# Performance work log

Hardware: AMD Instinct MI355X
Metric: run time of the kernel (lower is better)

## Reference

```python
import jax, jax.numpy as jnp
import numpy as np

B, S, IN, H, D, NH, L, C = 32, 512, 3, 64, 128, 8, 4, 5
NSUB = 10          # euler substeps per interval: dt = interval/10 for these inputs
MAX_CONSEC = 50    # max_consecutive_steps in torch code
DH = D // NH
EPS = 1e-5


def _ln(x, g, b):
    m = x.mean(-1, keepdims=True)
    v = ((x - m) ** 2).mean(-1, keepdims=True)
    return (x - m) / jnp.sqrt(v + EPS) * g + b


def setup_inputs():
    key = jax.random.key(0)
    ks = jax.random.split(key, 24)
    def g(i, shape, scale=0.05):
        return jax.random.normal(ks[i], shape, dtype=jnp.float32) * scale
    dts = jax.random.uniform(ks[0], (B, S), minval=0.001, maxval=0.05, dtype=jnp.float32)
    times = jnp.cumsum(dts, axis=1)  # strictly increasing, positive
    return dict(
        time_series=jax.random.normal(ks[1], (B, S, IN), dtype=jnp.float32),
        times=times,
        noise=jax.random.normal(ks[2], (S, NSUB, B, H), dtype=jnp.float32),
        mask=jnp.ones((B, S), dtype=bool),
        enc_w=g(3, (IN, H)), enc_b=jnp.zeros((H,)),
        enc_g=jnp.ones((H,)), enc_beta=jnp.zeros((H,)),
        dw1=g(4, (H + 1, 2 * H)), db1=jnp.zeros((2 * H,)),
        dw2=g(5, (2 * H, H)), db2=jnp.zeros((H,)),
        dw3=g(6, (H, H)), db3=jnp.zeros((H,)),
        aw1=g(7, (1, H)), ab1=jnp.zeros((H,)),
        aw2=g(8, (H, H)), ab2=jnp.zeros((H,)),
        bw1=g(9, (1, H)), bb1=jnp.zeros((H,)),
        bw2=g(10, (H, H)), bb2=jnp.zeros((H,)),
        min_diff=jnp.float32(0.1),
        in_w=g(11, (H, D)), in_b=jnp.zeros((D,)),
        wq=g(12, (L, D, D)), bq=jnp.zeros((L, D)),
        wk=g(13, (L, D, D)), bk=jnp.zeros((L, D)),
        wv=g(14, (L, D, D)), bv=jnp.zeros((L, D)),
        wo=g(15, (L, D, D)), bo=jnp.zeros((L, D)),
        ln1_g=jnp.ones((L, D)), ln1_b=jnp.zeros((L, D)),
        ln2_g=jnp.ones((L, D)), ln2_b=jnp.zeros((L, D)),
        fw1=g(16, (L, D, 4 * D)), fb1=jnp.zeros((L, 4 * D)),
        fw2=g(17, (L, 4 * D, D)), fb2=jnp.zeros((L, D)),
        cw1=g(18, (D, D // 2)), cb1=jnp.zeros((D // 2,)),
        cw2=g(19, (D // 2, C)), cb2=jnp.zeros((C,)),
    )


def reference(time_series, times, noise, mask, enc_w, enc_b, enc_g, enc_beta,
              dw1, db1, dw2, db2, dw3, db3, aw1, ab1, aw2, ab2, bw1, bb1, bw2, bb2,
              min_diff, in_w, in_b, wq, bq, wk, bk, wv, bv, wo, bo,
              ln1_g, ln1_b, ln2_g, ln2_b, fw1, fb1, fw2, fb2, cw1, cb1, cw2, cb2):
    # feature encoder: Linear -> LayerNorm -> ReLU (dropout off / eval)
    enc = jax.nn.relu(_ln(time_series @ enc_w + enc_b, enc_g, enc_beta))  # (B,S,H)

    def drift(t, y):
        tcol = jnp.full((y.shape[0], 1), t, dtype=y.dtype)
        ty = jnp.concatenate([y, tcol], axis=1)
        h1 = jnp.tanh(ty @ dw1 + db1)
        h2 = jnp.tanh(h1 @ dw2 + db2)
        return h2 @ dw3 + db3

    def diffusion(t, y):
        tcol = jnp.full((y.shape[0], 1), t, dtype=y.dtype)
        A = jax.nn.softplus(jnp.tanh(tcol @ aw1 + ab1) @ aw2 + ab2)
        Bt = jnp.tanh(jnp.tanh(tcol @ bw1 + bb1) @ bw2 + bb2)
        return A + Bt * y + jnp.abs(min_diff)

    t_seq = times[0]  # torch code uses batch element 0's timestamps for sdeint

    def step(carry, xs):
        state, consec = carry
        enc_i, t_prev, t_cur, dW = xs  # dW: (NSUB,B,H) standard normals
        h = (t_cur - t_prev) / NSUB    # dt = interval/10 (< self.dt for these inputs)
        sqh = jnp.sqrt(h)
        y0 = jax.lax.stop_gradient(state)  # torch detaches y0 at every step

        def sub(y, kw):
            k, dw = kw
            t = t_prev + k * h
            return y + drift(t, y) * h + diffusion(t, y) * sqh * dw, None

        y_int, _ = jax.lax.scan(sub, y0, (jnp.arange(NSUB, dtype=jnp.float32), dW))
        skip = consec >= MAX_CONSEC
        out = jnp.where(skip, enc_i, y_int)
        consec = jnp.where(skip, jnp.int32(0), consec + 1)
        return (out, consec), out

    y0 = enc[:, 0]
    xs = (jnp.swapaxes(enc, 0, 1)[1:], t_seq[:-1], t_seq[1:], noise[1:])
    _, traj = jax.lax.scan(step, (y0, jnp.int32(0)), xs)
    sde_features = jnp.concatenate([y0[:, None], jnp.swapaxes(traj, 0, 1)], axis=1)  # (B,S,H)

    mf = mask.astype(sde_features.dtype)
    sde_features = sde_features * mf[..., None]  # MaskedSequenceProcessor.apply_mask

    # ContiFormer (post-LN transformer encoder) over SDE features
    x = sde_features @ in_w + in_b  # (B,S,D)
    neg = jnp.asarray(-1e9, x.dtype)
    for l in range(L):
        q = (x @ wq[l] + bq[l]).reshape(B, S, NH, DH)
        k = (x @ wk[l] + bk[l]).reshape(B, S, NH, DH)
        v = (x @ wv[l] + bv[l]).reshape(B, S, NH, DH)
        scores = jnp.einsum('bqhd,bkhd->bhqk', q, k) / np.float32(np.sqrt(DH))
        scores = jnp.where(mask[:, None, None, :], scores, neg)
        att = jax.nn.softmax(scores, axis=-1)
        o = jnp.einsum('bhqk,bkhd->bqhd', att, v).reshape(B, S, D) @ wo[l] + bo[l]
        x = _ln(x + o, ln1_g[l], ln1_b[l])
        f = jax.nn.relu(x @ fw1[l] + fb1[l]) @ fw2[l] + fb2[l]
        x = _ln(x + f, ln2_g[l], ln2_b[l])
    pooled = (x * mf[..., None]).sum(1) / jnp.maximum(mf.sum(1, keepdims=True), 1.0)

    logits = jax.nn.relu(pooled @ cw1 + cb1) @ cw2 + cb2
    return logits, sde_features
```

## Files before the change

kernel.cpp:

```cpp
#include <hip/hip_runtime.h>
#include <hip/hip_bf16.h>


typedef __attribute__((ext_vector_type(8))) short short8;
typedef __attribute__((ext_vector_type(4))) float f32x4;

static constexpr int OFF_TS      = 0;
static constexpr int OFF_TIMES   = 49152;
static constexpr int OFF_ENCW    = 65536;
static constexpr int OFF_ENCB    = 65728;
static constexpr int OFF_ENCG    = 65792;
static constexpr int OFF_ENCBETA = 65856;
static constexpr int OFF_DW1     = 65920;
static constexpr int OFF_DB1     = 74240;
static constexpr int OFF_DW2     = 74368;
static constexpr int OFF_DB2     = 82560;
static constexpr int OFF_DW3     = 82624;
static constexpr int OFF_DB3     = 86720;
static constexpr int OFF_AW1     = 86784;
static constexpr int OFF_AB1     = 86848;
static constexpr int OFF_AW2     = 86912;
static constexpr int OFF_AB2     = 91008;
static constexpr int OFF_BW1     = 91072;
static constexpr int OFF_BB1     = 91136;
static constexpr int OFF_BW2     = 91200;
static constexpr int OFF_BB2     = 95296;
static constexpr int OFF_MD      = 95360;
static constexpr int OFF_INW     = 95424;
static constexpr int OFF_INB     = 103616;
static constexpr int OFF_WQ      = 103744;
static constexpr int OFF_BQ      = 169280;
static constexpr int OFF_WK      = 169792;
static constexpr int OFF_BK      = 235328;
static constexpr int OFF_WV      = 235840;
static constexpr int OFF_BV      = 301376;
static constexpr int OFF_WO      = 301888;
static constexpr int OFF_BO      = 367424;
static constexpr int OFF_LN1G    = 367936;
static constexpr int OFF_LN1B    = 368448;
static constexpr int OFF_LN2G    = 368960;
static constexpr int OFF_LN2B    = 369472;
static constexpr int OFF_FW1     = 369984;
static constexpr int OFF_FB1     = 632128;
static constexpr int OFF_FW2     = 634176;
static constexpr int OFF_FB2     = 896320;
static constexpr int OFF_CW1     = 896832;
static constexpr int OFF_CB1     = 905024;
static constexpr int OFF_CW2     = 905088;
static constexpr int OFF_CB2     = 905472;
static constexpr int OFF_FLAG    = 905536;
static constexpr int OFF_ENC     = 905600;
static constexpr int OFF_COEFA   = 3002752;
static constexpr int OFF_COEFB   = 3329792;
static constexpr int OFF_B1C     = 3656832;
static constexpr int OFF_X       = 4310912;
static constexpr int OFF_XBF     = 6408064;
static constexpr int OFF_QKVBF   = 7456640;
static constexpr int OFF_OBF     = 10602368;
static constexpr int OFF_HBF     = 11650944;
static constexpr int OFF_SDEBF   = 15845248;
static constexpr int OFF_WQKVT   = 16369536;
static constexpr int OFF_WOT     = 16467840;
static constexpr int OFF_FW1T    = 16500608;
static constexpr int OFF_FW2T    = 16631680;
static constexpr int OFF_INWT    = 16762752;
static constexpr int OFF_BQKV    = 16766848;
static constexpr int OFF_TMP     = 23185280;

struct PtrPack { const void* p[45]; };

__device__ inline float wsum64(float v) {
#pragma unroll
  for (int off = 32; off > 0; off >>= 1) v += __shfl_xor(v, off, 64);
  return v;
}

__device__ inline float fast_tanh(float x) {
  x = fminf(fmaxf(x, -15.f), 15.f);
  float e = __expf(2.f * x);
  return (e - 1.f) / (e + 1.f);
}

__device__ inline float tanh5(float x) {
  float e = __builtin_amdgcn_exp2f(x * 2.88539008f);
  return 1.f - 2.f * __builtin_amdgcn_rcpf(e + 1.f);
}

__device__ inline float bfdec(unsigned short h) {
  return __uint_as_float(((unsigned)h) << 16);
}

__device__ inline short f2bf(float f) {
  unsigned u = __float_as_uint(f);
  return (short)((u + 0x7FFFu + ((u >> 16) & 1u)) >> 16);
}

__device__ inline void lds_barrier() {
  asm volatile("s_waitcnt lgkmcnt(0)\ns_barrier" ::: "memory");
}

__global__ __launch_bounds__(256) void ingest_kernel(PtrPack pk, float* __restrict__ W) {
  const int NE = 43;
  const int cnt[NE] = {49152,16384,192,64,64,64,8320,128,8192,64,4096,64,64,64,4096,64,
                       64,64,4096,64,1,8192,128,65536,512,65536,512,65536,512,65536,512,
                       512,512,512,512,262144,2048,262144,512,8192,64,320,5};
  const int src[NE] = {0,1,4,5,6,7,8,9,10,11,12,13,14,15,16,17,18,19,20,21,22,23,24,
                       25,26,27,28,29,30,31,32,33,34,35,36,37,38,39,40,41,42,43,44};
  const int dst[NE] = {OFF_TS,OFF_TIMES,OFF_ENCW,OFF_ENCB,OFF_ENCG,OFF_ENCBETA,OFF_DW1,
                       OFF_DB1,OFF_DW2,OFF_DB2,OFF_DW3,OFF_DB3,OFF_AW1,OFF_AB1,OFF_AW2,
                       OFF_AB2,OFF_BW1,OFF_BB1,OFF_BW2,OFF_BB2,OFF_MD,OFF_INW,OFF_INB,
                       OFF_WQ,OFF_BQ,OFF_WK,OFF_BK,OFF_WV,OFF_BV,OFF_WO,OFF_BO,
                       OFF_LN1G,OFF_LN1B,OFF_LN2G,OFF_LN2B,OFF_FW1,OFF_FB1,OFF_FW2,
                       OFF_FB2,OFF_CW1,OFF_CB1,OFF_CW2,OFF_CB2};
  const unsigned* eg = (const unsigned*)pk.p[6];
  int gmode = (eg[0] == 0x3F803F80u) ? 1 : 0;

  __shared__ int isbf[NE];
  if (threadIdx.x < NE) {
    int k = threadIdx.x;
    int f = gmode;
    if (gmode) {
      const unsigned short* us = (const unsigned short*)pk.p[src[k]];
      int n = cnt[k] < 32 ? cnt[k] : 32;
      for (int i = 0; i < n; ++i) {
        unsigned short h = us[i];
        if (h & 0x7FFF) {
          float a = fabsf(bfdec(h));
          if (!(a > 1e-20f && a < 1e4f)) { f = 0; break; }
        }
      }
    }
    isbf[k] = f;
  }
  __syncthreads();

  int gid = blockIdx.x * 256 + threadIdx.x;
  int stride = gridDim.x * 256;
  if (gid == 0) {
    int nf = gmode;
    if (gmode) {
      const unsigned short* us = (const unsigned short*)pk.p[2];
      for (int i = 0; i < 32; ++i) {
        unsigned short h = us[i];
        if (h & 0x7FFF) {
          float a = fabsf(bfdec(h));
          if (!(a > 1e-20f && a < 1e4f)) { nf = 0; break; }
        }
      }
    }
    ((int*)W)[OFF_FLAG] = nf;
  }
  for (int k = 0; k < NE; ++k) {
    int n = cnt[k];
    float* dp = W + dst[k];
    if (isbf[k]) {
      const unsigned short* us = (const unsigned short*)pk.p[src[k]];
      for (int e = gid; e < n; e += stride) dp[e] = bfdec(us[e]);
    } else {
      const float* fs = (const float*)pk.p[src[k]];
      for (int e = gid; e < n; e += stride) dp[e] = fs[e];
    }
  }
}

__global__ __launch_bounds__(128) void prelude_kernel(float* __restrict__ W,
                                                      float* __restrict__ outf) {
  int blk = blockIdx.x;
  int tid = threadIdx.x;
  if (blk < 5110) {
    int bi = blk;
    int step = bi / 10, k = bi - step * 10;
    float t_prev = W[OFF_TIMES + step];
    float t_cur  = W[OFF_TIMES + step + 1];
    float h = (t_cur - t_prev) * 0.1f;
    float t = t_prev + (float)k * h;
    __shared__ float av[64], bv[64];
    if (tid < 64) av[tid] = fast_tanh(t * W[OFF_AW1 + tid] + W[OFF_AB1 + tid]);
    else { int j = tid - 64; bv[j] = fast_tanh(t * W[OFF_BW1 + j] + W[OFF_BB1 + j]); }
    __syncthreads();
    if (tid < 64) {
      float a = W[OFF_AB2 + tid];
      for (int i = 0; i < 64; ++i) a += av[i] * W[OFF_AW2 + i*64 + tid];
      W[OFF_COEFA + bi*64 + tid] = fmaxf(a, 0.f) + log1pf(__expf(-fabsf(a)));
    } else {
      int j = tid - 64;
      float a = W[OFF_BB2 + j];
      for (int i = 0; i < 64; ++i) a += bv[i] * W[OFF_BW2 + i*64 + j];
      W[OFF_COEFB + bi*64 + j] = fast_tanh(a);
    }
    W[OFF_B1C + bi*128 + tid] = t * W[OFF_DW1 + 64*128 + tid] + W[OFF_DB1 + tid];
  } else if (blk < 5462) {
    if (tid >= 64) return;
    int idx = blk - 5110;
    int b = idx / 11, gi = idx - b*11;
    int row = b*512 + gi*51;
    int j = tid;
    float t0 = W[OFF_TS + row*3 + 0];
    float t1 = W[OFF_TS + row*3 + 1];
    float t2 = W[OFF_TS + row*3 + 2];
    float v = W[OFF_ENCB + j] + t0 * W[OFF_ENCW + j] + t1 * W[OFF_ENCW + 64 + j]
            + t2 * W[OFF_ENCW + 128 + j];
    float mean = wsum64(v) * (1.f / 64.f);
    float d = v - mean;
    float var = wsum64(d * d) * (1.f / 64.f);
    float o = d * rsqrtf(var + 1e-5f) * W[OFF_ENCG + j] + W[OFF_ENCBETA + j];
    o = fmaxf(o, 0.f);
    W[OFF_ENC + row*64 + j] = o;
    ((short*)(W + OFF_SDEBF))[row*64 + j] = f2bf(o);
    outf[160 + row*64 + j] = o;
  } else {
    short* wqkvT = (short*)(W + OFF_WQKVT);
    short* woT   = (short*)(W + OFF_WOT);
    short* fw1T  = (short*)(W + OFF_FW1T);
    short* fw2T  = (short*)(W + OFF_FW2T);
    short* inwT  = (short*)(W + OFF_INWT);
    float* bqkv  = W + OFF_BQKV;
    int gid = (blk - 5462) * 128 + tid;
    int stride = 512 * 128;
    for (int e = gid; e < 4096; e += stride) W[OFF_TMP + e] = 0.f;
    for (int e = gid; e < 796160; e += stride) {
      if (e < 196608) {
        int l = e / 49152, r = e % 49152, n = r >> 7, k = r & 127;
        float v = (n < 128) ? W[OFF_WQ + l*16384 + k*128 + n]
                : (n < 256) ? W[OFF_WK + l*16384 + k*128 + (n - 128)]
                            : W[OFF_WV + l*16384 + k*128 + (n - 256)];
        wqkvT[e] = f2bf(v);
      } else if (e < 262144) {
        int t = e - 196608; int l = t / 16384, r = t % 16384, n = r >> 7, k = r & 127;
        woT[t] = f2bf(W[OFF_WO + l*16384 + k*128 + n]);
      } else if (e < 524288) {
        int t = e - 262144; int l = t / 65536, r = t % 65536, n = r >> 7, k = r & 127;
        fw1T[t] = f2bf(W[OFF_FW1 + l*65536 + k*512 + n]);
      } else if (e < 786432) {
        int t = e - 524288; int l = t / 65536, r = t % 65536, n = r >> 9, k = r & 511;
        fw2T[t] = f2bf(W[OFF_FW2 + l*65536 + k*128 + n]);
      } else if (e < 794624) {
        int t = e - 786432; int n = t >> 6, k = t & 63;
        inwT[t] = f2bf(W[OFF_INW + k*128 + n]);
      } else {
        int t = e - 794624; int l = t / 384, j = t % 384;
        bqkv[t] = (j < 128) ? W[OFF_BQ + l*128 + j]
                : (j < 256) ? W[OFF_BK + l*128 + (j - 128)]
                            : W[OFF_BV + l*128 + (j - 256)];
      }
    }
  }
}

__global__ __launch_bounds__(256, 1) void sde_kernel(float* __restrict__ W,
                                                     const void* __restrict__ noise,
                                                     float* __restrict__ outf) {
  __shared__ short ybf[16 * 72];
  __shared__ short h1bf[16 * 136];
  __shared__ short h2bf[16 * 72];

  const int tid = threadIdx.x;
  const int w   = tid >> 6;
  const int lane = tid & 63;
  const int q   = lane >> 4;
  const int lq  = lane & 15;
  const int g   = blockIdx.x >> 1;
  const int r0  = (blockIdx.x & 1) * 16;

  const int nmode = ((const int*)W)[OFF_FLAG];
  const float md = fabsf(W[OFF_MD]);
  const unsigned short* nb16 = (const unsigned short*)noise;
  const float* nf32 = (const float*)noise;
  short* sdebf = (short*)(W + OFF_SDEBF);

  const int ncol = w*16 + lq;
  short8 B1f[2][2];
#pragma unroll
  for (int kt = 0; kt < 2; ++kt)
#pragma unroll
    for (int ct = 0; ct < 2; ++ct)
#pragma unroll
      for (int j = 0; j < 8; ++j)
        B1f[kt][ct][j] = f2bf(W[OFF_DW1 + (kt*32 + q*8 + j)*128 + w*32 + ct*16 + lq]);
  short8 B2f[4];
#pragma unroll
  for (int kt = 0; kt < 4; ++kt)
#pragma unroll
    for (int j = 0; j < 8; ++j)
      B2f[kt][j] = f2bf(W[OFF_DW2 + (kt*32 + q*8 + j)*64 + ncol]);
  short8 B3f[2];
#pragma unroll
  for (int kt = 0; kt < 2; ++kt)
#pragma unroll
    for (int j = 0; j < 8; ++j)
      B3f[kt][j] = f2bf(W[OFF_DW3 + (kt*32 + q*8 + j)*64 + ncol]);
  const float db2v = W[OFF_DB2 + ncol];
  const float db3v = W[OFF_DB3 + ncol];

  float yreg[4];
#pragma unroll
  for (int r = 0; r < 4; ++r) {
    yreg[r] = W[OFF_ENC + ((r0 + q*4 + r)*512 + 51*g)*64 + ncol];
    ybf[(q*4 + r)*72 + ncol] = f2bf(yreg[r]);
  }

  const int ci0 = 51*g*10;
  float bias_a = W[OFF_B1C + ci0*128 + w*32 + lq];
  float bias_b = W[OFF_B1C + ci0*128 + w*32 + 16 + lq];
  float ca = W[OFF_COEFA + ci0*64 + ncol];
  float cb = W[OFF_COEFB + ci0*64 + ncol];

  const int nsteps = (g == 10) ? 1 : 50;
  for (int m = 0; m < nsteps; ++m) {
    const int istep = 51*g + m;
    const float t_prev = W[OFF_TIMES + istep];
    const float t_cur  = W[OFF_TIMES + istep + 1];
    const float hstep = (t_cur - t_prev) * 0.1f;
    const float sqh = sqrtf(hstep);
    for (int k = 0; k < 10; ++k) {
      const int ci = istep*10 + k;
      const int cin = (ci + 1 > 5109) ? 5109 : ci + 1;
      float b1na = W[OFF_B1C + cin*128 + w*32 + lq];
      float b1nb = W[OFF_B1C + cin*128 + w*32 + 16 + lq];
      float can = W[OFF_COEFA + cin*64 + ncol];
      float cbn = W[OFF_COEFB + cin*64 + ncol];
      float dwv[4];
      {
        const int nb = (((istep + 1)*10 + k)*32 + r0 + q*4)*64 + ncol;
#pragma unroll
        for (int r = 0; r < 4; ++r)
          dwv[r] = nmode ? bfdec(nb16[nb + r*64]) : nf32[nb + r*64];
      }
      lds_barrier();
      {
        short8 a0 = *(const short8*)&ybf[lq*72 + q*8];
        short8 a1 = *(const short8*)&ybf[lq*72 + 32 + q*8];
        f32x4 c0 = {bias_a, bias_a, bias_a, bias_a};
        c0 = __builtin_amdgcn_mfma_f32_16x16x32_bf16(a0, B1f[0][0], c0, 0, 0, 0);
        c0 = __builtin_amdgcn_mfma_f32_16x16x32_bf16(a1, B1f[1][0], c0, 0, 0, 0);
        f32x4 c1 = {bias_b, bias_b, bias_b, bias_b};
        c1 = __builtin_amdgcn_mfma_f32_16x16x32_bf16(a0, B1f[0][1], c1, 0, 0, 0);
        c1 = __builtin_amdgcn_mfma_f32_16x16x32_bf16(a1, B1f[1][1], c1, 0, 0, 0);
#pragma unroll
        for (int r = 0; r < 4; ++r) {
          h1bf[(q*4 + r)*136 + w*32 + lq]      = f2bf(tanh5(c0[r]));
          h1bf[(q*4 + r)*136 + w*32 + 16 + lq] = f2bf(tanh5(c1[r]));
        }
      }
      lds_barrier();
      {
        short8 h0 = *(const short8*)&h1bf[lq*136 + q*8];
        short8 h1 = *(const short8*)&h1bf[lq*136 + 32 + q*8];
        short8 h2 = *(const short8*)&h1bf[lq*136 + 64 + q*8];
        short8 h3 = *(const short8*)&h1bf[lq*136 + 96 + q*8];
        f32x4 cA = {db2v, db2v, db2v, db2v};
        cA = __builtin_amdgcn_mfma_f32_16x16x32_bf16(h0, B2f[0], cA, 0, 0, 0);
        cA = __builtin_amdgcn_mfma_f32_16x16x32_bf16(h1, B2f[1], cA, 0, 0, 0);
        f32x4 cB = {0.f, 0.f, 0.f, 0.f};
        cB = __builtin_amdgcn_mfma_f32_16x16x32_bf16(h2, B2f[2], cB, 0, 0, 0);
        cB = __builtin_amdgcn_mfma_f32_16x16x32_bf16(h3, B2f[3], cB, 0, 0, 0);
#pragma unroll
        for (int r = 0; r < 4; ++r)
          h2bf[(q*4 + r)*72 + ncol] = f2bf(tanh5(cA[r] + cB[r]));
      }
      lds_barrier();
      {
        short8 g0 = *(const short8*)&h2bf[lq*72 + q*8];
        short8 g1 = *(const short8*)&h2bf[lq*72 + 32 + q*8];
        f32x4 d = {db3v, db3v, db3v, db3v};
        d = __builtin_amdgcn_mfma_f32_16x16x32_bf16(g0, B3f[0], d, 0, 0, 0);
        d = __builtin_amdgcn_mfma_f32_16x16x32_bf16(g1, B3f[1], d, 0, 0, 0);
#pragma unroll
        for (int r = 0; r < 4; ++r) {
          float yv = yreg[r];
          yv = yv + d[r]*hstep + (ca + cb*yv + md)*sqh*dwv[r];
          yreg[r] = yv;
          ybf[(q*4 + r)*72 + ncol] = f2bf(yv);
        }
      }
      bias_a = b1na; bias_b = b1nb; ca = can; cb = cbn;
    }
#pragma unroll
    for (int r = 0; r < 4; ++r) {
      const int gi = ((r0 + q*4 + r)*512 + (istep + 1))*64 + ncol;
      sdebf[gi] = f2bf(yreg[r]);
      outf[160 + gi] = yreg[r];
    }
  }
}

__global__ __launch_bounds__(256) void gemm_ln64_kernel(
    const short* __restrict__ A, const short* __restrict__ BT,
    const float* __restrict__ bias, float* __restrict__ X,
    short* __restrict__ Xb, int K) {
  __shared__ short As[64 * 40];
  __shared__ short Bs[128 * 40];
  const int tid = threadIdx.x;
  const int w = tid >> 6, lane = tid & 63, q = lane >> 4, lq = lane & 15;
  const int bm = blockIdx.x * 64;
  f32x4 acc[8];
#pragma unroll
  for (int i = 0; i < 8; ++i) acc[i] = (f32x4){0.f, 0.f, 0.f, 0.f};

  const int arow = tid >> 2, acol = (tid & 3) * 8;
  const int brow = tid >> 1, bcol = (tid & 1) * 16;
  for (int k0 = 0; k0 < K; k0 += 32) {
    short8 a  = *(const short8*)&A[(bm + arow)*K + k0 + acol];
    short8 b0 = *(const short8*)&BT[brow*K + k0 + bcol];
    short8 b1 = *(const short8*)&BT[brow*K + k0 + bcol + 8];
    __syncthreads();
    *(short8*)&As[arow*40 + acol]    = a;
    *(short8*)&Bs[brow*40 + bcol]    = b0;
    *(short8*)&Bs[brow*40 + bcol+8]  = b1;
    __syncthreads();
    short8 af = *(const short8*)&As[(w*16 + lq)*40 + q*8];
#pragma unroll
    for (int ni = 0; ni < 8; ++ni) {
      short8 bf = *(const short8*)&Bs[(ni*16 + lq)*40 + q*8];
      acc[ni] = __builtin_amdgcn_mfma_f32_16x16x32_bf16(af, bf, acc[ni], 0, 0, 0);
    }
  }
#pragma unroll
  for (int r = 0; r < 4; ++r) {
    const int row = bm + w*16 + q*4 + r;
#pragma unroll
    for (int ni = 0; ni < 8; ++ni) {
      const int col = ni*16 + lq;
      float v = acc[ni][r] + bias[col];
      X[row*128 + col] = v;
      Xb[row*128 + col] = f2bf(v);
    }
  }
}

__global__ __launch_bounds__(512, 4) void ffn_fused_kernel(
    const short* __restrict__ Obf, const short* __restrict__ woT,
    const float* __restrict__ bo,
    const float* __restrict__ ln1g, const float* __restrict__ ln1b,
    const short* __restrict__ fw1T, const float* __restrict__ fb1,
    const short* __restrict__ fw2T, const float* __restrict__ fb2,
    const float* __restrict__ ln2g, const float* __restrict__ ln2b,
    float* __restrict__ X, short* __restrict__ Xb,
    float* __restrict__ psum) {
  __shared__ short U1[32 * 136];
  __shared__ short Hs[32 * 136];
  __shared__ short Bs[128 * 136];
  __shared__ float LNp[32][4][2];
  const int tid = threadIdx.x;
  const int w8 = tid >> 6, rg = w8 & 1, cq = w8 >> 1;
  const int lane = tid & 63, q = lane >> 4, lq = lane & 15;
  const int bm = blockIdx.x * 32;
  const int sr = tid >> 4, sc = (tid & 15) * 8;
  const int bn = tid >> 2, kb = (tid & 3) * 32;
  const int rowl0 = rg*16 + q*4;

  short8 abuf, bbuf[4];
  abuf = *(const short8*)&Obf[(bm + sr)*128 + sc];
#pragma unroll
  for (int j = 0; j < 4; ++j)
    bbuf[j] = *(const short8*)&woT[bn*128 + kb + j*8];
  *(short8*)&U1[sr*136 + sc] = abuf;
#pragma unroll
  for (int j = 0; j < 4; ++j) *(short8*)&Bs[bn*136 + kb + j*8] = bbuf[j];
  lds_barrier();

#pragma unroll
  for (int j = 0; j < 4; ++j)
    bbuf[j] = *(const short8*)&fw1T[bn*128 + kb + j*8];

  f32x4 acc[2];
#pragma unroll
  for (int i = 0; i < 2; ++i) acc[i] = (f32x4){0.f, 0.f, 0.f, 0.f};
#pragma unroll
  for (int ks = 0; ks < 4; ++ks) {
    short8 af = *(const short8*)&U1[(rg*16 + lq)*136 + ks*32 + q*8];
#pragma unroll
    for (int ni = 0; ni < 2; ++ni) {
      short8 bf = *(const short8*)&Bs[((cq*2 + ni)*16 + lq)*136 + ks*32 + q*8];
      acc[ni] = __builtin_amdgcn_mfma_f32_16x16x32_bf16(af, bf, acc[ni], 0, 0, 0);
    }
  }
  float vbuf[4][2];
#pragma unroll
  for (int r = 0; r < 4; ++r) {
    const int row = bm + rowl0 + r;
    float s = 0.f, s2 = 0.f;
#pragma unroll
    for (int ni = 0; ni < 2; ++ni) {
      const int col = cq*32 + ni*16 + lq;
      float t = acc[ni][r] + bo[col] + X[row*128 + col];
      vbuf[r][ni] = t; s += t; s2 += t*t;
    }
#pragma unroll
    for (int off = 1; off < 16; off <<= 1) {
      s  += __shfl_xor(s, off, 16);
      s2 += __shfl_xor(s2, off, 16);
    }
    if (lq == 0) { LNp[rowl0 + r][cq][0] = s; LNp[rowl0 + r][cq][1] = s2; }
  }
  lds_barrier();
#pragma unroll
  for (int j = 0; j < 4; ++j) *(short8*)&Bs[bn*136 + kb + j*8] = bbuf[j];
#pragma unroll
  for (int j = 0; j < 4; ++j)
    bbuf[j] = *(const short8*)&fw2T[bn*512 + kb + j*8];
  float xv[4][2];
#pragma unroll
  for (int r = 0; r < 4; ++r) {
    const int rowl = rowl0 + r;
    float s  = LNp[rowl][0][0] + LNp[rowl][1][0] + LNp[rowl][2][0] + LNp[rowl][3][0];
    float s2 = LNp[rowl][0][1] + LNp[rowl][1][1] + LNp[rowl][2][1] + LNp[rowl][3][1];
    float mean = s * (1.f / 128.f);
    float var = s2 * (1.f / 128.f) - mean * mean;
    float inv = rsqrtf(var + 1e-5f);
#pragma unroll
    for (int ni = 0; ni < 2; ++ni) {
      const int col = cq*32 + ni*16 + lq;
      float o = (vbuf[r][ni] - mean) * inv * ln1g[col] + ln1b[col];
      xv[r][ni] = o;
      U1[rowl*136 + col] = f2bf(o);
    }
  }
  lds_barrier();

  f32x4 acc2[2];
#pragma unroll
  for (int i = 0; i < 2; ++i) acc2[i] = (f32x4){0.f, 0.f, 0.f, 0.f};

  for (int c = 0; c < 4; ++c) {
#pragma unroll
    for (int i = 0; i < 2; ++i) acc[i] = (f32x4){0.f, 0.f, 0.f, 0.f};
#pragma unroll
    for (int ks = 0; ks < 4; ++ks) {
      short8 af = *(const short8*)&U1[(rg*16 + lq)*136 + ks*32 + q*8];
#pragma unroll
      for (int ni = 0; ni < 2; ++ni) {
        short8 bf = *(const short8*)&Bs[((cq*2 + ni)*16 + lq)*136 + ks*32 + q*8];
        acc[ni] = __builtin_amdgcn_mfma_f32_16x16x32_bf16(af, bf, acc[ni], 0, 0, 0);
      }
    }
#pragma unroll
    for (int r = 0; r < 4; ++r)
#pragma unroll
      for (int ni = 0; ni < 2; ++ni) {
        const int cl = cq*32 + ni*16 + lq;
        float hvv = fmaxf(acc[ni][r] + fb1[c*128 + cl], 0.f);
        Hs[(rowl0 + r)*136 + cl] = f2bf(hvv);
      }
    lds_barrier();
#pragma unroll
    for (int j = 0; j < 4; ++j) *(short8*)&Bs[bn*136 + kb + j*8] = bbuf[j];
    if (c < 3) {
#pragma unroll
      for (int j = 0; j < 4; ++j)
        bbuf[j] = *(const short8*)&fw1T[((c + 1)*128 + bn)*128 + kb + j*8];
    }
    lds_barrier();
#pragma unroll
    for (int ks = 0; ks < 4; ++ks) {
      short8 af = *(const short8*)&Hs[(rg*16 + lq)*136 + ks*32 + q*8];
#pragma unroll
      for (int ni = 0; ni < 2; ++ni) {
        short8 bf = *(const short8*)&Bs[((cq*2 + ni)*16 + lq)*136 + ks*32 + q*8];
        acc2[ni] = __builtin_amdgcn_mfma_f32_16x16x32_bf16(af, bf, acc2[ni], 0, 0, 0);
      }
    }
    if (c < 3) {
      lds_barrier();
#pragma unroll
      for (int j = 0; j < 4; ++j) *(short8*)&Bs[bn*136 + kb + j*8] = bbuf[j];
#pragma unroll
      for (int j = 0; j < 4; ++j)
        bbuf[j] = *(const short8*)&fw2T[bn*512 + (c + 1)*128 + kb + j*8];
      lds_barrier();
    }
  }

#pragma unroll
  for (int r = 0; r < 4; ++r) {
    float s = 0.f, s2 = 0.f;
#pragma unroll
    for (int ni = 0; ni < 2; ++ni) {
      const int col = cq*32 + ni*16 + lq;
      float t = acc2[ni][r] + fb2[col] + xv[r][ni];
      vbuf[r][ni] = t; s += t; s2 += t*t;
    }
#pragma unroll
    for (int off = 1; off < 16; off <<= 1) {
      s  += __shfl_xor(s, off, 16);
      s2 += __shfl_xor(s2, off, 16);
    }
    if (lq == 0) { LNp[rowl0 + r][cq][0] = s; LNp[rowl0 + r][cq][1] = s2; }
  }
  lds_barrier();
  float ps[2] = {0.f, 0.f};
#pragma unroll
  for (int r = 0; r < 4; ++r) {
    const int rowl = rowl0 + r;
    const int row = bm + rowl;
    float s  = LNp[rowl][0][0] + LNp[rowl][1][0] + LNp[rowl][2][0] + LNp[rowl][3][0];
    float s2 = LNp[rowl][0][1] + LNp[rowl][1][1] + LNp[rowl][2][1] + LNp[rowl][3][1];
    float mean = s * (1.f / 128.f);
    float var = s2 * (1.f / 128.f) - mean * mean;
    float inv = rsqrtf(var + 1e-5f);
#pragma unroll
    for (int ni = 0; ni < 2; ++ni) {
      const int col = cq*32 + ni*16 + lq;
      float o = (vbuf[r][ni] - mean) * inv * ln2g[col] + ln2b[col];
      X[row*128 + col] = o;
      Xb[row*128 + col] = f2bf(o);
      ps[ni] += o;
    }
  }
  if (psum != nullptr) {
    const int b = bm >> 9;
#pragma unroll
    for (int ni = 0; ni < 2; ++ni) {
      float v = ps[ni];
      v += __shfl_xor(v, 16, 64);
      v += __shfl_xor(v, 32, 64);
      if (q == 0) atomicAdd(&psum[b*128 + cq*32 + ni*16 + lq], v);
    }
  }
}

__global__ __launch_bounds__(512, 4) void attn_fused_kernel(
    const short* __restrict__ Xb, const short* __restrict__ wqkvT,
    const float* __restrict__ bqkv, short* __restrict__ O) {
  __shared__ short Kt[512 * 20];
  __shared__ short Vt[16 * 520];
  __shared__ short U[8 * 2176];
  __shared__ short Qt[8 * 320];
  const int blk = blockIdx.x;
  const int qg = blk & 1, bh = blk >> 1;
  const int h = bh & 7, b = bh >> 3;
  const int tid = threadIdx.x;
  const int w = tid >> 6, lane = tid & 63, q = lane >> 4, lq = lane & 15;

  const float qb = bqkv[h*16 + lq];
  const float kb = bqkv[128 + h*16 + lq];
  const float vb = bqkv[256 + h*16 + lq];

  short* Uw = &U[w * 2176];
  const int srow = lane >> 2;
  const int scol = (lane & 3) * 32;
  {
    short8 BKf[4], BVf[4];
#pragma unroll
    for (int ks = 0; ks < 4; ++ks) {
      BKf[ks] = *(const short8*)&wqkvT[(128 + h*16 + lq)*128 + ks*32 + q*8];
      BVf[ks] = *(const short8*)&wqkvT[(256 + h*16 + lq)*128 + ks*32 + q*8];
    }
    for (int sub = 0; sub < 4; ++sub) {
      const int grow = b*512 + w*64 + sub*16;
      short8 xa[4];
#pragma unroll
      for (int j = 0; j < 4; ++j)
        xa[j] = *(const short8*)&Xb[(size_t)(grow + srow)*128 + scol + j*8];
#pragma unroll
      for (int j = 0; j < 4; ++j)
        *(short8*)&Uw[srow*136 + scol + j*8] = xa[j];
      f32x4 kacc = {0.f, 0.f, 0.f, 0.f};
      f32x4 vacc = {0.f, 0.f, 0.f, 0.f};
#pragma unroll
      for (int ks = 0; ks < 4; ++ks) {
        short8 af = *(const short8*)&Uw[lq*136 + ks*32 + q*8];
        kacc = __builtin_amdgcn_mfma_f32_16x16x32_bf16(af, BKf[ks], kacc, 0, 0, 0);
        vacc = __builtin_amdgcn_mfma_f32_16x16x32_bf16(af, BVf[ks], vacc, 0, 0, 0);
      }
#pragma unroll
      for (int r = 0; r < 4; ++r) {
        const int key = w*64 + sub*16 + q*4 + r;
        Kt[key*20 + lq]  = f2bf(kacc[r] + kb);
        Vt[lq*520 + key] = f2bf(vacc[r] + vb);
      }
    }
  }
  lds_barrier();

  short* Pw = Uw;
  short* Qw = &Qt[w * 320];
  const float cexp = 0.25f * 1.44269504f;

  for (int qi = 0; qi < 2; ++qi) {
    const int qrow0 = b*512 + (qg*16 + w*2 + qi)*16;
    {
      short8 BQf[4];
#pragma unroll
      for (int ks = 0; ks < 4; ++ks)
        BQf[ks] = *(const short8*)&wqkvT[(h*16 + lq)*128 + ks*32 + q*8];
      f32x4 qacc = {0.f, 0.f, 0.f, 0.f};
#pragma unroll
      for (int ks = 0; ks < 4; ++ks) {
        short8 af = *(const short8*)&Xb[(size_t)(qrow0 + lq)*128 + ks*32 + q*8];
        qacc = __builtin_amdgcn_mfma_f32_16x16x32_bf16(af, BQf[ks], qacc, 0, 0, 0);
      }
#pragma unroll
      for (int r = 0; r < 4; ++r)
        Qw[(q*4 + r)*20 + lq] = f2bf(qacc[r] + qb);
    }
    short8 aq = (short8){0,0,0,0,0,0,0,0};
    if (q < 2) aq = *(const short8*)&Qw[lq*20 + q*8];

    float mx[4] = {-1e30f, -1e30f, -1e30f, -1e30f};
    float ls[4] = {0.f, 0.f, 0.f, 0.f};
    f32x4 o = {0.f, 0.f, 0.f, 0.f};
#pragma unroll
    for (int p = 0; p < 2; ++p) {
      f32x4 acc[16];
#pragma unroll
      for (int t = 0; t < 16; ++t) {
        short8 bk = (short8){0,0,0,0,0,0,0,0};
        if (q < 2) bk = *(const short8*)&Kt[((p*16 + t)*16 + lq)*20 + q*8];
        f32x4 z = {0.f, 0.f, 0.f, 0.f};
        acc[t] = __builtin_amdgcn_mfma_f32_16x16x32_bf16(aq, bk, z, 0, 0, 0);
      }
      float lm[4] = {-1e30f, -1e30f, -1e30f, -1e30f};
#pragma unroll
      for (int t = 0; t < 16; ++t)
#pragma unroll
        for (int r = 0; r < 4; ++r) lm[r] = fmaxf(lm[r], acc[t][r]);
#pragma unroll
      for (int off = 1; off < 16; off <<= 1)
#pragma unroll
        for (int r = 0; r < 4; ++r) lm[r] = fmaxf(lm[r], __shfl_xor(lm[r], off, 16));
      float mnew[4], scl[4], lsum[4];
#pragma unroll
      for (int r = 0; r < 4; ++r) {
        mnew[r] = fmaxf(mx[r], lm[r]);
        scl[r] = __builtin_amdgcn_exp2f((mx[r] - mnew[r]) * cexp);
        lsum[r] = 0.f;
      }
#pragma unroll
      for (int t = 0; t < 16; ++t)
#pragma unroll
        for (int r = 0; r < 4; ++r) {
          float pv = __builtin_amdgcn_exp2f((acc[t][r] - mnew[r]) * cexp);
          acc[t][r] = pv;
          lsum[r] += pv;
        }
#pragma unroll
      for (int r = 0; r < 4; ++r) {
        ls[r] = ls[r] * scl[r] + lsum[r];
        o[r] *= scl[r];
        mx[r] = mnew[r];
      }
#pragma unroll
      for (int c = 0; c < 2; ++c) {
#pragma unroll
        for (int tt = 0; tt < 8; ++tt)
#pragma unroll
          for (int r = 0; r < 4; ++r)
            Pw[(q*4 + r)*136 + tt*16 + lq] =
                (short)(__float_as_uint(acc[c*8 + tt][r]) >> 16);
#pragma unroll
        for (int kk = 0; kk < 4; ++kk) {
          short8 ap = *(const short8*)&Pw[lq*136 + kk*32 + q*8];
          short8 bv = *(const short8*)&Vt[lq*520 + p*256 + c*128 + kk*32 + q*8];
          o = __builtin_amdgcn_mfma_f32_16x16x32_bf16(ap, bv, o, 0, 0, 0);
        }
      }
    }
#pragma unroll
    for (int off = 1; off < 16; off <<= 1)
#pragma unroll
      for (int r = 0; r < 4; ++r) ls[r] += __shfl_xor(ls[r], off, 16);
#pragma unroll
    for (int r = 0; r < 4; ++r) {
      float ov = o[r] * __builtin_amdgcn_rcpf(ls[r]);
      O[(size_t)(qrow0 + q*4 + r)*128 + h*16 + lq] = f2bf(ov);
    }
  }
}

__global__ __launch_bounds__(128) void pool_cls_kernel(const float* __restrict__ W,
                                                       float* __restrict__ outf) {
  int b = blockIdx.x, j = threadIdx.x;
  __shared__ float pooled[128];
  __shared__ float hid[64];
  pooled[j] = W[OFF_TMP + b*128 + j] * (1.f / 512.f);
  __syncthreads();
  if (j < 64) {
    float a = W[OFF_CB1 + j];
    for (int i = 0; i < 128; ++i) a += pooled[i] * W[OFF_CW1 + i*64 + j];
    hid[j] = fmaxf(a, 0.f);
  }
  __syncthreads();
  if (j < 5) {
    float a = W[OFF_CB2 + j];
    for (int i = 0; i < 64; ++i) a += hid[i] * W[OFF_CW2 + i*5 + j];
    outf[b*5 + j] = a;
  }
}

extern "C" void kernel_launch(void* const* d_in, const int* in_sizes, int n_in,
                              void* d_out, int out_size, void* d_ws, size_t ws_size,
                              hipStream_t stream) {
  (void)in_sizes; (void)out_size; (void)ws_size;
  float* W = reinterpret_cast<float*>(d_ws);
  float* outf = reinterpret_cast<float*>(d_out);
  short* sdebf = (short*)(W + OFF_SDEBF);
  short* xbf   = (short*)(W + OFF_XBF);
  short* obf   = (short*)(W + OFF_OBF);
  PtrPack pk;
  for (int i = 0; i < 45 && i < n_in; ++i) pk.p[i] = d_in[i];

  ingest_kernel<<<512, 256, 0, stream>>>(pk, W);
  prelude_kernel<<<5974, 128, 0, stream>>>(W, outf);
  sde_kernel<<<22, 256, 0, stream>>>(W, d_in[2], outf);

  gemm_ln64_kernel<<<256, 256, 0, stream>>>(sdebf, (short*)(W + OFF_INWT),
      W + OFF_INB, W + OFF_X, xbf, 64);
  for (int l = 0; l < 4; ++l) {
    attn_fused_kernel<<<512, 512, 0, stream>>>(xbf,
        (short*)(W + OFF_WQKVT) + l*49152, W + OFF_BQKV + l*384, obf);
    ffn_fused_kernel<<<512, 512, 0, stream>>>(obf,
        (short*)(W + OFF_WOT) + l*16384, W + OFF_BO + l*128,
        W + OFF_LN1G + l*128, W + OFF_LN1B + l*128,
        (short*)(W + OFF_FW1T) + l*65536, W + OFF_FB1 + l*512,
        (short*)(W + OFF_FW2T) + l*65536, W + OFF_FB2 + l*128,
        W + OFF_LN2G + l*128, W + OFF_LN2B + l*128,
        W + OFF_X, xbf, (l == 3) ? (W + OFF_TMP) : nullptr);
  }
  pool_cls_kernel<<<32, 128, 0, stream>>>(W, outf);
}
```

Baseline: 980.1 us.

## Enlarge attention and FFN tiles; single-pass softmax over all keys

The attention kernel now has one block per (batch, head) instead of two, so the K/V projection over the 512 keys is computed once rather than twice. Softmax switches from a two-chunk online form to a single pass holding all 32 score tiles in registers. The FFN kernel runs 1024 threads over 64-row tiles, halving the per-thread weight staging and sharing each weight tile across more rows. The cost is higher register pressure (32 accumulator tiles, launch bound lowered to 2) and fewer blocks in the grid, which may reduce occupancy.

Result: faster. 865.2 us, median of 2 (-11.7%).

```diff
diff --git a/kernel.cpp b/kernel.cpp
--- a/kernel.cpp
+++ b/kernel.cpp
@@ -428,7 +428,7 @@
   }
 }
 
-__global__ __launch_bounds__(512, 4) void ffn_fused_kernel(
+__global__ __launch_bounds__(1024, 4) void ffn_fused_kernel(
     const short* __restrict__ Obf, const short* __restrict__ woT,
     const float* __restrict__ bo,
     const float* __restrict__ ln1g, const float* __restrict__ ln1b,
@@ -437,30 +437,30 @@
     const float* __restrict__ ln2g, const float* __restrict__ ln2b,
     float* __restrict__ X, short* __restrict__ Xb,
     float* __restrict__ psum) {
-  __shared__ short U1[32 * 136];
-  __shared__ short Hs[32 * 136];
+  __shared__ short U1[64 * 136];
+  __shared__ short Hs[64 * 136];
   __shared__ short Bs[128 * 136];
-  __shared__ float LNp[32][4][2];
+  __shared__ float LNp[64][4][2];
   const int tid = threadIdx.x;
-  const int w8 = tid >> 6, rg = w8 & 1, cq = w8 >> 1;
+  const int w16 = tid >> 6, rg = w16 & 3, cq = w16 >> 2;
   const int lane = tid & 63, q = lane >> 4, lq = lane & 15;
-  const int bm = blockIdx.x * 32;
+  const int bm = blockIdx.x * 64;
   const int sr = tid >> 4, sc = (tid & 15) * 8;
-  const int bn = tid >> 2, kb = (tid & 3) * 32;
+  const int bn = tid >> 3, kb = (tid & 7) * 16;
   const int rowl0 = rg*16 + q*4;
 
-  short8 abuf, bbuf[4];
+  short8 abuf, bbuf[2];
   abuf = *(const short8*)&Obf[(bm + sr)*128 + sc];
 #pragma unroll
-  for (int j = 0; j < 4; ++j)
+  for (int j = 0; j < 2; ++j)
     bbuf[j] = *(const short8*)&woT[bn*128 + kb + j*8];
   *(short8*)&U1[sr*136 + sc] = abuf;
 #pragma unroll
-  for (int j = 0; j < 4; ++j) *(short8*)&Bs[bn*136 + kb + j*8] = bbuf[j];
+  for (int j = 0; j < 2; ++j) *(short8*)&Bs[bn*136 + kb + j*8] = bbuf[j];
   lds_barrier();
 
 #pragma unroll
-  for (int j = 0; j < 4; ++j)
+  for (int j = 0; j < 2; ++j)
     bbuf[j] = *(const short8*)&fw1T[bn*128 + kb + j*8];
 
   f32x4 acc[2];
@@ -495,9 +495,9 @@
   }
   lds_barrier();
 #pragma unroll
-  for (int j = 0; j < 4; ++j) *(short8*)&Bs[bn*136 + kb + j*8] = bbuf[j];
-#pragma unroll
-  for (int j = 0; j < 4; ++j)
+  for (int j = 0; j < 2; ++j) *(short8*)&Bs[bn*136 + kb + j*8] = bbuf[j];
+#pragma unroll
+  for (int j = 0; j < 2; ++j)
     bbuf[j] = *(const short8*)&fw2T[bn*512 + kb + j*8];
   float xv[4][2];
 #pragma unroll
@@ -544,10 +544,10 @@
       }
     lds_barrier();
 #pragma unroll
-    for (int j = 0; j < 4; ++j) *(short8*)&Bs[bn*136 + kb + j*8] = bbuf[j];
+    for (int j = 0; j < 2; ++j) *(short8*)&Bs[bn*136 + kb + j*8] = bbuf[j];
     if (c < 3) {
 #pragma unroll
-      for (int j = 0; j < 4; ++j)
+      for (int j = 0; j < 2; ++j)
         bbuf[j] = *(const short8*)&fw1T[((c + 1)*128 + bn)*128 + kb + j*8];
     }
     lds_barrier();
@@ -563,9 +563,9 @@
     if (c < 3) {
       lds_barrier();
 #pragma unroll
-      for (int j = 0; j < 4; ++j) *(short8*)&Bs[bn*136 + kb + j*8] = bbuf[j];
-#pragma unroll
-      for (int j = 0; j < 4; ++j)
+      for (int j = 0; j < 2; ++j) *(short8*)&Bs[bn*136 + kb + j*8] = bbuf[j];
+#pragma unroll
+      for (int j = 0; j < 2; ++j)
         bbuf[j] = *(const short8*)&fw2T[bn*512 + (c + 1)*128 + kb + j*8];
       lds_barrier();
     }
@@ -619,7 +619,7 @@
   }
 }
 
-__global__ __launch_bounds__(512, 4) void attn_fused_kernel(
+__global__ __launch_bounds__(512, 2) void attn_fused_kernel(
     const short* __restrict__ Xb, const short* __restrict__ wqkvT,
     const float* __restrict__ bqkv, short* __restrict__ O) {
   __shared__ short Kt[512 * 20];
@@ -627,11 +627,17 @@
   __shared__ short U[8 * 2176];
   __shared__ short Qt[8 * 320];
   const int blk = blockIdx.x;
-  const int qg = blk & 1, bh = blk >> 1;
-  const int h = bh & 7, b = bh >> 3;
+  const int h = blk & 7, b = blk >> 3;
   const int tid = threadIdx.x;
   const int w = tid >> 6, lane = tid & 63, q = lane >> 4, lq = lane & 15;
 
+  short8 BQf[4], BKf[4], BVf[4];
+#pragma unroll
+  for (int ks = 0; ks < 4; ++ks) {
+    BQf[ks] = *(const short8*)&wqkvT[(h*16 + lq)*128 + ks*32 + q*8];
+    BKf[ks] = *(const short8*)&wqkvT[(128 + h*16 + lq)*128 + ks*32 + q*8];
+    BVf[ks] = *(const short8*)&wqkvT[(256 + h*16 + lq)*128 + ks*32 + q*8];
+  }
   const float qb = bqkv[h*16 + lq];
   const float kb = bqkv[128 + h*16 + lq];
   const float vb = bqkv[256 + h*16 + lq];
@@ -639,36 +645,28 @@
   short* Uw = &U[w * 2176];
   const int srow = lane >> 2;
   const int scol = (lane & 3) * 32;
-  {
-    short8 BKf[4], BVf[4];
+  for (int sub = 0; sub < 4; ++sub) {
+    const int grow = b*512 + w*64 + sub*16;
+    short8 xa[4];
+#pragma unroll
+    for (int j = 0; j < 4; ++j)
+      xa[j] = *(const short8*)&Xb[(size_t)(grow + srow)*128 + scol + j*8];
+#pragma unroll
+    for (int j = 0; j < 4; ++j)
+      *(short8*)&Uw[srow*136 + scol + j*8] = xa[j];
+    f32x4 kacc = {0.f, 0.f, 0.f, 0.f};
+    f32x4 vacc = {0.f, 0.f, 0.f, 0.f};
 #pragma unroll
     for (int ks = 0; ks < 4; ++ks) {
-      BKf[ks] = *(const short8*)&wqkvT[(128 + h*16 + lq)*128 + ks*32 + q*8];
-      BVf[ks] = *(const short8*)&wqkvT[(256 + h*16 + lq)*128 + ks*32 + q*8];
-    }
-    for (int sub = 0; sub < 4; ++sub) {
-      const int grow = b*512 + w*64 + sub*16;
-      short8 xa[4];
-#pragma unroll
-      for (int j = 0; j < 4; ++j)
-        xa[j] = *(const short8*)&Xb[(size_t)(grow + srow)*128 + scol + j*8];
-#pragma unroll
-      for (int j = 0; j < 4; ++j)
-        *(short8*)&Uw[srow*136 + scol + j*8] = xa[j];
-      f32x4 kacc = {0.f, 0.f, 0.f, 0.f};
-      f32x4 vacc = {0.f, 0.f, 0.f, 0.f};
-#pragma unroll
-      for (int ks = 0; ks < 4; ++ks) {
-        short8 af = *(const short8*)&Uw[lq*136 + ks*32 + q*8];
-        kacc = __builtin_amdgcn_mfma_f32_16x16x32_bf16(af, BKf[ks], kacc, 0, 0, 0);
-        vacc = __builtin_amdgcn_mfma_f32_16x16x32_bf16(af, BVf[ks], vacc, 0, 0, 0);
-      }
-#pragma unroll
-      for (int r = 0; r < 4; ++r) {
-        const int key = w*64 + sub*16 + q*4 + r;
-        Kt[key*20 + lq]  = f2bf(kacc[r] + kb);
-        Vt[lq*520 + key] = f2bf(vacc[r] + vb);
-      }
+      short8 af = *(const short8*)&Uw[lq*136 + ks*32 + q*8];
+      kacc = __builtin_amdgcn_mfma_f32_16x16x32_bf16(af, BKf[ks], kacc, 0, 0, 0);
+      vacc = __builtin_amdgcn_mfma_f32_16x16x32_bf16(af, BVf[ks], vacc, 0, 0, 0);
+    }
+#pragma unroll
+    for (int r = 0; r < 4; ++r) {
+      const int key = w*64 + sub*16 + q*4 + r;
+      Kt[key*20 + lq]  = f2bf(kacc[r] + kb);
+      Vt[lq*520 + key] = f2bf(vacc[r] + vb);
     }
   }
   lds_barrier();
@@ -677,13 +675,9 @@
   short* Qw = &Qt[w * 320];
   const float cexp = 0.25f * 1.44269504f;
 
-  for (int qi = 0; qi < 2; ++qi) {
-    const int qrow0 = b*512 + (qg*16 + w*2 + qi)*16;
+  for (int qi = 0; qi < 4; ++qi) {
+    const int qrow0 = b*512 + (w*4 + qi)*16;
     {
-      short8 BQf[4];
-#pragma unroll
-      for (int ks = 0; ks < 4; ++ks)
-        BQf[ks] = *(const short8*)&wqkvT[(h*16 + lq)*128 + ks*32 + q*8];
       f32x4 qacc = {0.f, 0.f, 0.f, 0.f};
 #pragma unroll
       for (int ks = 0; ks < 4; ++ks) {
@@ -697,69 +691,53 @@
     short8 aq = (short8){0,0,0,0,0,0,0,0};
     if (q < 2) aq = *(const short8*)&Qw[lq*20 + q*8];
 
+    f32x4 acc[32];
+#pragma unroll
+    for (int t = 0; t < 32; ++t) {
+      short8 bk = (short8){0,0,0,0,0,0,0,0};
+      if (q < 2) bk = *(const short8*)&Kt[(t*16 + lq)*20 + q*8];
+      f32x4 z = {0.f, 0.f, 0.f, 0.f};
+      acc[t] = __builtin_amdgcn_mfma_f32_16x16x32_bf16(aq, bk, z, 0, 0, 0);
+    }
     float mx[4] = {-1e30f, -1e30f, -1e30f, -1e30f};
+#pragma unroll
+    for (int t = 0; t < 32; ++t)
+#pragma unroll
+      for (int r = 0; r < 4; ++r) mx[r] = fmaxf(mx[r], acc[t][r]);
+#pragma unroll
+    for (int off = 1; off < 16; off <<= 1)
+#pragma unroll
+      for (int r = 0; r < 4; ++r) mx[r] = fmaxf(mx[r], __shfl_xor(mx[r], off, 16));
     float ls[4] = {0.f, 0.f, 0.f, 0.f};
+#pragma unroll
+    for (int t = 0; t < 32; ++t)
+#pragma unroll
+      for (int r = 0; r < 4; ++r) {
+        float p = __builtin_amdgcn_exp2f((acc[t][r] - mx[r]) * cexp);
+        acc[t][r] = p;
+        ls[r] += p;
+      }
+#pragma unroll
+    for (int off = 1; off < 16; off <<= 1)
+#pragma unroll
+      for (int r = 0; r < 4; ++r) ls[r] += __shfl_xor(ls[r], off, 16);
+
     f32x4 o = {0.f, 0.f, 0.f, 0.f};
 #pragma unroll
-    for (int p = 0; p < 2; ++p) {
-      f32x4 acc[16];
-#pragma unroll
-      for (int t = 0; t < 16; ++t) {
-        short8 bk = (short8){0,0,0,0,0,0,0,0};
-        if (q < 2) bk = *(const short8*)&Kt[((p*16 + t)*16 + lq)*20 + q*8];
-        f32x4 z = {0.f, 0.f, 0.f, 0.f};
-        acc[t] = __builtin_amdgcn_mfma_f32_16x16x32_bf16(aq, bk, z, 0, 0, 0);
-      }
-      float lm[4] = {-1e30f, -1e30f, -1e30f, -1e30f};
-#pragma unroll
-      for (int t = 0; t < 16; ++t)
-#pragma unroll
-        for (int r = 0; r < 4; ++r) lm[r] = fmaxf(lm[r], acc[t][r]);
-#pragma unroll
-      for (int off = 1; off < 16; off <<= 1)
-#pragma unroll
-        for (int r = 0; r < 4; ++r) lm[r] = fmaxf(lm[r], __shfl_xor(lm[r], off, 16));
-      float mnew[4], scl[4], lsum[4];
-#pragma unroll
-      for (int r = 0; r < 4; ++r) {
-        mnew[r] = fmaxf(mx[r], lm[r]);
-        scl[r] = __builtin_amdgcn_exp2f((mx[r] - mnew[r]) * cexp);
-        lsum[r] = 0.f;
-      }
-#pragma unroll
-      for (int t = 0; t < 16; ++t)
-#pragma unroll
-        for (int r = 0; r < 4; ++r) {
-          float pv = __builtin_amdgcn_exp2f((acc[t][r] - mnew[r]) * cexp);
-          acc[t][r] = pv;
-          lsum[r] += pv;
-        }
-#pragma unroll
-      for (int r = 0; r < 4; ++r) {
-        ls[r] = ls[r] * scl[r] + lsum[r];
-        o[r] *= scl[r];
-        mx[r] = mnew[r];
-      }
-#pragma unroll
-      for (int c = 0; c < 2; ++c) {
-#pragma unroll
-        for (int tt = 0; tt < 8; ++tt)
-#pragma unroll
-          for (int r = 0; r < 4; ++r)
-            Pw[(q*4 + r)*136 + tt*16 + lq] =
-                (short)(__float_as_uint(acc[c*8 + tt][r]) >> 16);
-#pragma unroll
-        for (int kk = 0; kk < 4; ++kk) {
-          short8 ap = *(const short8*)&Pw[lq*136 + kk*32 + q*8];
-          short8 bv = *(const short8*)&Vt[lq*520 + p*256 + c*128 + kk*32 + q*8];
-          o = __builtin_amdgcn_mfma_f32_16x16x32_bf16(ap, bv, o, 0, 0, 0);
-        }
-      }
-    }
-#pragma unroll
-    for (int off = 1; off < 16; off <<= 1)
-#pragma unroll
-      for (int r = 0; r < 4; ++r) ls[r] += __shfl_xor(ls[r], off, 16);
+    for (int c = 0; c < 4; ++c) {
+#pragma unroll
+      for (int tt = 0; tt < 8; ++tt)
+#pragma unroll
+        for (int r = 0; r < 4; ++r)
+          Pw[(q*4 + r)*136 + tt*16 + lq] =
+              (short)(__float_as_uint(acc[c*8 + tt][r]) >> 16);
+#pragma unroll
+      for (int kk = 0; kk < 4; ++kk) {
+        short8 ap = *(const short8*)&Pw[lq*136 + kk*32 + q*8];
+        short8 bv = *(const short8*)&Vt[lq*520 + c*128 + kk*32 + q*8];
+        o = __builtin_amdgcn_mfma_f32_16x16x32_bf16(ap, bv, o, 0, 0, 0);
+      }
+    }
 #pragma unroll
     for (int r = 0; r < 4; ++r) {
       float ov = o[r] * __builtin_amdgcn_rcpf(ls[r]);
@@ -807,9 +785,9 @@
   gemm_ln64_kernel<<<256, 256, 0, stream>>>(sdebf, (short*)(W + OFF_INWT),
       W + OFF_INB, W + OFF_X, xbf, 64);
   for (int l = 0; l < 4; ++l) {
-    attn_fused_kernel<<<512, 512, 0, stream>>>(xbf,
+    attn_fused_kernel<<<256, 512, 0, stream>>>(xbf,
         (short*)(W + OFF_WQKVT) + l*49152, W + OFF_BQKV + l*384, obf);
-    ffn_fused_kernel<<<512, 512, 0, stream>>>(obf,
+    ffn_fused_kernel<<<256, 1024, 0, stream>>>(obf,
         (short*)(W + OFF_WOT) + l*16384, W + OFF_BO + l*128,
         W + OFF_LN1G + l*128, W + OFF_LN1B + l*128,
         (short*)(W + OFF_FW1T) + l*65536, W + OFF_FB1 + l*512,
```
